# Performance work log

Hardware: AMD Instinct MI355X
Metric: run time of the kernel (lower is better)

## Reference

```python
import jax, jax.numpy as jnp
import numpy as np

B, S, D = 4, 2048, 1024
H = 16
HD = D // H

def setup_inputs() -> dict:
    key = jax.random.key(0)
    ks = jax.random.split(key, 6)
    s = 0.02
    return {
        "input_tensor": jax.random.normal(ks[0], (B, S, D), dtype=jnp.float32),
        "Wq": jax.random.normal(ks[1], (D, D), dtype=jnp.float32) * s,
        "Wk": jax.random.normal(ks[2], (D, D), dtype=jnp.float32) * s,
        "Wv": jax.random.normal(ks[3], (D, D), dtype=jnp.float32) * s,
        "Wo": jax.random.normal(ks[4], (D, D), dtype=jnp.float32) * s,
        "bo": jax.random.normal(ks[5], (D,), dtype=jnp.float32) * s,
    }

def reference(input_tensor, Wq, Wk, Wv, Wo, bo):
    b, n, _ = input_tensor.shape
    # projections (nn.Linear: x @ W.T; bias=False for qkv)
    q = jnp.einsum('bnd,ed->bne', input_tensor, Wq).reshape(b, n, H, HD).transpose(0, 2, 1, 3)
    k = jnp.einsum('bnd,ed->bne', input_tensor, Wk).reshape(b, n, H, HD).transpose(0, 2, 1, 3)
    v = jnp.einsum('bnd,ed->bne', input_tensor, Wv).reshape(b, n, H, HD).transpose(0, 2, 1, 3)
    scores = jnp.einsum('bhqd,bhkd->bhqk', q, k)  # [B,H,S,S]
    causal = jnp.triu(jnp.ones((n, n), dtype=bool), k=1)
    scores = jnp.where(causal, -jnp.inf, scores)
    weights = jax.nn.softmax(scores / jnp.sqrt(jnp.float32(HD)), axis=-1)
    ctx = jnp.einsum('bhqk,bhkd->bhqd', weights, v)  # [B,H,S,HD]
    ctx = ctx.transpose(0, 2, 1, 3).reshape(b, n, D)
    return jnp.einsum('bnd,ed->bne', ctx, Wo) + bo
```

## Files before the change

kernel.cpp:

```cpp
#include <hip/hip_runtime.h>
#include <stdint.h>

#define S_LEN 2048
#define DIM   1024
#define NH    16
#define HD    64
#define BATCH 4
#define M_ROWS (BATCH * S_LEN)

typedef __attribute__((ext_vector_type(8))) __bf16 bf16x8;
typedef __attribute__((ext_vector_type(4))) float  f32x4;

union Frag { bf16x8 v; uint4 q; };

__device__ __forceinline__ ushort f2bf(float f) {
  union { float f; unsigned u; } x; x.f = f;
  unsigned r = x.u + 0x7fffu + ((x.u >> 16) & 1u);
  return (ushort)(r >> 16);
}
__device__ __forceinline__ ushort f2bf_n(float f) {
  union { __bf16 b; ushort u; } x; x.b = (__bf16)f; return x.u;
}

__device__ __forceinline__ f32x4 mfma16(const Frag& a, const Frag& b, f32x4 c) {
  return __builtin_amdgcn_mfma_f32_16x16x32_bf16(a.v, b.v, c, 0, 0, 0);
}

__device__ __forceinline__ void gld_lds16(const ushort* g, ushort* l) {
  __builtin_amdgcn_global_load_lds(
      (__attribute__((address_space(1))) void*)g,
      (__attribute__((address_space(3))) void*)l, 16, 0, 0);
}

__global__ void cast_x_kernel(const float* __restrict__ src, ushort* __restrict__ dst) {
  int i = blockIdx.x * 256 + threadIdx.x;
  float4 f = ((const float4*)src)[i];
  ushort4 u; u.x = f2bf(f.x); u.y = f2bf(f.y); u.z = f2bf(f.z); u.w = f2bf(f.w);
  ((ushort4*)dst)[i] = u;
}

__global__ void cast_w_kernel(const float* __restrict__ w0, const float* __restrict__ w1,
                              const float* __restrict__ w2, const float* __restrict__ w3,
                              ushort* __restrict__ d0, ushort* __restrict__ d1,
                              ushort* __restrict__ d2, ushort* __restrict__ d3) {
  const float* s; ushort* d;
  int z = blockIdx.y;
  if (z == 0) { s = w0; d = d0; } else if (z == 1) { s = w1; d = d1; }
  else if (z == 2) { s = w2; d = d2; } else { s = w3; d = d3; }
  int i = blockIdx.x * 256 + threadIdx.x;
  float4 f = ((const float4*)s)[i];
  ushort4 u; u.x = f2bf(f.x); u.y = f2bf(f.y); u.z = f2bf(f.z); u.w = f2bf(f.w);
  ((ushort4*)d)[i] = u;
}

template <int MODE>
__global__ __launch_bounds__(256)
void gemm_bk64(const ushort* __restrict__ A,
               const ushort* __restrict__ B0, const ushort* __restrict__ B1,
               const ushort* __restrict__ B2,
               ushort* __restrict__ Qb, ushort* __restrict__ Kb, ushort* __restrict__ Vtb,
               float* __restrict__ outf, const float* __restrict__ bias, float scaleq) {
  __shared__ __align__(16) ushort As[128 * 64];
  __shared__ __align__(16) ushort Bs[128 * 64];
  const int K = DIM;
  int lane = threadIdx.x & 63, wave = threadIdx.x >> 6;
  int quad = lane >> 4, l15 = lane & 15;

  const int GX = (MODE == 0) ? 24 : 8;
  int lin = blockIdx.x + GX * blockIdx.y;
  int xcd = lin & 7, idx = lin >> 3;
  int by = xcd * 8 + idx / GX;
  int bx = idx % GX;

  int rowBase = by * 128;
  int wsel, colBase;
  const ushort* Bt;
  if (MODE == 0) {
    wsel = bx >> 3;
    colBase = (bx & 7) * 128;
    Bt = (wsel == 0) ? B0 : (wsel == 1) ? B1 : B2;
  } else {
    wsel = 0;
    colBase = bx * 128;
    Bt = B0;
  }
  int wm = (wave >> 1) * 64, wn = (wave & 1) * 64;

  const ushort* Ag = A + (size_t)rowBase * K;
  const ushort* Bg = Bt + (size_t)colBase * K;

  f32x4 acc[4][4];
#pragma unroll
  for (int i = 0; i < 4; i++)
#pragma unroll
    for (int j = 0; j < 4; j++) acc[i][j] = (f32x4){0.f, 0.f, 0.f, 0.f};

  for (int k0 = 0; k0 < K; k0 += 64) {
#pragma unroll
    for (int cc = 0; cc < 4; ++cc) {
      int c = wave * 4 + cc;
      int s = c * 64 + lane;
      int row = s >> 3;
      int c8 = (s & 7) ^ (row & 7);
      gld_lds16(Ag + (size_t)row * K + k0 + c8 * 8, &As[c * 512]);
      gld_lds16(Bg + (size_t)row * K + k0 + c8 * 8, &Bs[c * 512]);
    }
    __syncthreads();
    Frag af[4][2], bf[4][2];
#pragma unroll
    for (int t = 0; t < 4; t++) {
      int ar = wm + t * 16 + l15;
      int br = wn + t * 16 + l15;
#pragma unroll
      for (int kk = 0; kk < 2; kk++) {
        af[t][kk].q = *(const uint4*)&As[ar * 64 + (((kk * 4 + quad) ^ (ar & 7))) * 8];
        bf[t][kk].q = *(const uint4*)&Bs[br * 64 + (((kk * 4 + quad) ^ (br & 7))) * 8];
      }
    }
#pragma unroll
    for (int kk = 0; kk < 2; kk++)
#pragma unroll
      for (int i = 0; i < 4; i++)
#pragma unroll
        for (int j = 0; j < 4; j++) acc[i][j] = mfma16(af[i][kk], bf[j][kk], acc[i][j]);
    __syncthreads();
  }

#pragma unroll
  for (int i = 0; i < 4; i++) {
    int rowt = wm + i * 16 + quad * 4;
#pragma unroll
    for (int j = 0; j < 4; j++) {
      int e = colBase + wn + j * 16 + l15;
      if (MODE == 0) {
        if (wsel < 2) {
          ushort* dst = wsel ? Kb : Qb;
          float sc = wsel ? 1.f : scaleq;
#pragma unroll
          for (int r = 0; r < 4; r++) {
            size_t m = (size_t)(rowBase + rowt + r);
            dst[m * DIM + e] = f2bf(acc[i][j][r] * sc);
          }
        } else {
          int h = e >> 6, hd = e & 63;
          int m0 = rowBase + rowt;
          int b = m0 >> 11, s0 = m0 & (S_LEN - 1);
          ushort4 u;
          u.x = f2bf(acc[i][j][0]); u.y = f2bf(acc[i][j][1]);
          u.z = f2bf(acc[i][j][2]); u.w = f2bf(acc[i][j][3]);
          *(ushort4*)&Vtb[((size_t)((b * NH + h) * HD + hd) << 11) + s0] = u;
        }
      } else {
        float bv = bias[e];
#pragma unroll
        for (int r = 0; r < 4; r++) {
          int m = rowBase + rowt + r;
          outf[(size_t)m * DIM + e] = acc[i][j][r] + bv;
        }
      }
    }
  }
}

__global__ __launch_bounds__(256)
void flash_attn(const ushort* __restrict__ Qb, const ushort* __restrict__ Kb,
                const ushort* __restrict__ Vtb, ushort* __restrict__ Ctx) {
  __shared__ __align__(16) ushort Ks[128 * 64];
  __shared__ __align__(16) ushort Vs[64 * 128];

  int lane = threadIdx.x & 63, wave = threadIdx.x >> 6;
  int quad = lane >> 4, l15 = lane & 15;
  int bh = blockIdx.x;
  int qt = (gridDim.y - 1) - blockIdx.y;
  int q0 = qt * 128, wq0 = wave * 32;
  int b = bh >> 4, h = bh & 15;

  const ushort* Qg = Qb + (size_t)b * S_LEN * DIM + h * HD;
  const ushort* Kg = Kb + (size_t)b * S_LEN * DIM + h * HD;
  const ushort* Vh = Vtb + (size_t)bh * HD * S_LEN;

#pragma unroll
  for (int cc = 0; cc < 4; ++cc) {
    int c = wave * 4 + cc;
    int s = c * 64 + lane;
    int row = s >> 3;
    int c8 = (s & 7) ^ (row & 7);
    gld_lds16(Qg + (size_t)(q0 + row) * DIM + c8 * 8, &Ks[c * 512]);
  }
  __syncthreads();
  Frag qf[2][2];
#pragma unroll
  for (int it = 0; it < 2; ++it)
#pragma unroll
    for (int ks = 0; ks < 2; ++ks) {
      int row = wq0 + it * 16 + l15;
      int c8 = (ks * 4 + quad) ^ (row & 7);
      qf[it][ks].q = *(const uint4*)&Ks[row * 64 + c8 * 8];
    }
  __syncthreads();

  float lst[2] = {0.f, 0.f};
  f32x4 oacc[2][4];
#pragma unroll
  for (int it = 0; it < 2; ++it)
#pragma unroll
    for (int dt = 0; dt < 4; ++dt) oacc[it][dt] = (f32x4){0.f, 0.f, 0.f, 0.f};

  ushort* Pw = &Ks[wave * 2048];

  for (int kt = 0; kt <= qt; ++kt) {
#pragma unroll
    for (int cc = 0; cc < 4; ++cc) {
      int c = wave * 4 + cc;
      int s = c * 64 + lane;
      int krow = s >> 3;
      int kc8 = (s & 7) ^ (krow & 7);
      gld_lds16(Kg + (size_t)(kt * 128 + krow) * DIM + kc8 * 8, &Ks[c * 512]);
      int vrow = s >> 4;
      int vc8 = (s & 15) ^ (vrow & 15);
      gld_lds16(Vh + (size_t)vrow * S_LEN + kt * 128 + vc8 * 8, &Vs[c * 512]);
    }
    __syncthreads();

    f32x4 sacc[2][8];
#pragma unroll
    for (int jt = 0; jt < 8; ++jt) {
      int row = jt * 16 + l15;
      Frag kf0, kf1;
      kf0.q = *(const uint4*)&Ks[row * 64 + ((quad) ^ (row & 7)) * 8];
      kf1.q = *(const uint4*)&Ks[row * 64 + ((4 + quad) ^ (row & 7)) * 8];
#pragma unroll
      for (int it = 0; it < 2; ++it) {
        f32x4 a = (f32x4){0.f, 0.f, 0.f, 0.f};
        a = mfma16(kf0, qf[it][0], a);
        a = mfma16(kf1, qf[it][1], a);
        sacc[it][jt] = a;
      }
    }
    __syncthreads();

    if (kt == qt) {
#pragma unroll
      for (int it = 0; it < 2; ++it)
#pragma unroll
        for (int jt = 0; jt < 8; ++jt)
#pragma unroll
          for (int r = 0; r < 4; ++r)
            if (jt * 16 + quad * 4 + r > wq0 + it * 16 + l15)
              sacc[it][jt][r] = -1e30f;
    }

#pragma unroll
    for (int it = 0; it < 2; ++it) {
      float ps = 0.f;
#pragma unroll
      for (int jt = 0; jt < 8; ++jt) {
        float p0 = exp2f(sacc[it][jt][0]);
        float p1 = exp2f(sacc[it][jt][1]);
        float p2 = exp2f(sacc[it][jt][2]);
        float p3 = exp2f(sacc[it][jt][3]);
        ps += (p0 + p1) + (p2 + p3);
        ushort4 u; u.x = f2bf_n(p0); u.y = f2bf_n(p1); u.z = f2bf_n(p2); u.w = f2bf_n(p3);
        int cw = (jt * 4 + quad) ^ (l15 << 1);
        *(ushort4*)&Pw[l15 * 128 + cw * 4] = u;
      }
      ps += __shfl_xor(ps, 16);
      ps += __shfl_xor(ps, 32);
      lst[it] += ps;

      Frag pf[4];
#pragma unroll
      for (int ks = 0; ks < 4; ++ks) {
        int cr = (ks * 8 + quad * 2) ^ (l15 << 1);
        pf[ks].q = *(const uint4*)&Pw[l15 * 128 + cr * 4];
      }

#pragma unroll
      for (int dt = 0; dt < 4; ++dt) {
        f32x4 a = oacc[it][dt];
#pragma unroll
        for (int ks = 0; ks < 4; ++ks) {
          int row = dt * 16 + l15;
          Frag vf;
          vf.q = *(const uint4*)&Vs[row * 128 + (((ks * 4 + quad) ^ (row & 15))) * 8];
          a = mfma16(pf[ks], vf, a);
        }
        oacc[it][dt] = a;
      }
    }
    __syncthreads();
  }

#pragma unroll
  for (int it = 0; it < 2; ++it) {
    float linv = 1.f / lst[it];
    float lr[4];
#pragma unroll
    for (int r = 0; r < 4; ++r) lr[r] = __shfl(linv, quad * 4 + r);
#pragma unroll
    for (int r = 0; r < 4; ++r) {
      int qg = q0 + wq0 + it * 16 + quad * 4 + r;
      size_t base = ((size_t)(b * S_LEN + qg)) * DIM + h * HD;
#pragma unroll
      for (int dt = 0; dt < 4; ++dt)
        Ctx[base + dt * 16 + l15] = f2bf_n(oacc[it][dt][r] * lr[r]);
    }
  }
}

extern "C" void kernel_launch(void* const* d_in, const int* in_sizes, int n_in,
                              void* d_out, int out_size, void* d_ws, size_t ws_size,
                              hipStream_t stream) {
  (void)in_sizes; (void)n_in; (void)out_size; (void)ws_size;
  const float* x  = (const float*)d_in[0];
  const float* Wq = (const float*)d_in[1];
  const float* Wk = (const float*)d_in[2];
  const float* Wv = (const float*)d_in[3];
  const float* Wo = (const float*)d_in[4];
  const float* bo = (const float*)d_in[5];
  float* out = (float*)d_out;

  ushort* Xb  = (ushort*)d_ws;
  ushort* Wqb = Xb  + (size_t)M_ROWS * DIM;
  ushort* Wkb = Wqb + (size_t)DIM * DIM;
  ushort* Wvb = Wkb + (size_t)DIM * DIM;
  ushort* Wob = Wvb + (size_t)DIM * DIM;
  ushort* Qb  = Wob + (size_t)DIM * DIM;
  ushort* Kb  = Qb  + (size_t)M_ROWS * DIM;
  ushort* Vtb = Kb  + (size_t)M_ROWS * DIM;
  ushort* Ctx = Vtb + (size_t)M_ROWS * DIM;

  const float SCALE_Q = 0.18033688011112042f;

  cast_x_kernel<<<dim3(M_ROWS * DIM / 1024), 256, 0, stream>>>(x, Xb);
  cast_w_kernel<<<dim3(DIM * DIM / 1024, 4), 256, 0, stream>>>(Wq, Wk, Wv, Wo, Wqb, Wkb, Wvb, Wob);

  gemm_bk64<0><<<dim3(24, 64), 256, 0, stream>>>(Xb, Wqb, Wkb, Wvb, Qb, Kb, Vtb,
                                                 nullptr, nullptr, SCALE_Q);

  flash_attn<<<dim3(BATCH * NH, S_LEN / 128), 256, 0, stream>>>(Qb, Kb, Vtb, Ctx);

  gemm_bk64<1><<<dim3(8, 64), 256, 0, stream>>>(Ctx, Wob, nullptr, nullptr, nullptr, nullptr,
                                                nullptr, out, bo, 1.0f);
}
```

Before: 269.3 us.

## Pair causal query tiles per block, add dedicated P buffer, vectorize GEMM stores

The attention kernel now processes two query tiles per block (tile i and its mirror NQT-1-i), so every block does equal causal work; the grid is halved to match. P moves to its own padded shared buffer, which lets the mid-iteration barrier between the QK and PV phases be removed. The GEMM swaps MFMA operand order for the Q/K and output paths so each lane holds contiguous columns, allowing 4-wide vector stores and float4 bias loads. The changes trade more LDS per block and fewer blocks against better load balance and fewer synchronisations and store instructions.

```diff
diff --git a/kernel.cpp b/kernel.cpp
--- a/kernel.cpp
+++ b/kernel.cpp
@@ -7,6 +7,7 @@
 #define HD    64
 #define BATCH 4
 #define M_ROWS (BATCH * S_LEN)
+#define PSTR  136
 
 typedef __attribute__((ext_vector_type(8))) __bf16 bf16x8;
 typedef __attribute__((ext_vector_type(4))) float  f32x4;
@@ -85,6 +86,7 @@
     Bt = B0;
   }
   int wm = (wave >> 1) * 64, wn = (wave & 1) * 64;
+  bool swapT = (MODE == 1) || (wsel < 2);
 
   const ushort* Ag = A + (size_t)rowBase * K;
   const ushort* Bg = Bt + (size_t)colBase * K;
@@ -117,46 +119,67 @@
         bf[t][kk].q = *(const uint4*)&Bs[br * 64 + (((kk * 4 + quad) ^ (br & 7))) * 8];
       }
     }
-#pragma unroll
-    for (int kk = 0; kk < 2; kk++)
-#pragma unroll
-      for (int i = 0; i < 4; i++)
-#pragma unroll
-        for (int j = 0; j < 4; j++) acc[i][j] = mfma16(af[i][kk], bf[j][kk], acc[i][j]);
+    if (swapT) {
+#pragma unroll
+      for (int kk = 0; kk < 2; kk++)
+#pragma unroll
+        for (int i = 0; i < 4; i++)
+#pragma unroll
+          for (int j = 0; j < 4; j++) acc[i][j] = mfma16(bf[j][kk], af[i][kk], acc[i][j]);
+    } else {
+#pragma unroll
+      for (int kk = 0; kk < 2; kk++)
+#pragma unroll
+        for (int i = 0; i < 4; i++)
+#pragma unroll
+          for (int j = 0; j < 4; j++) acc[i][j] = mfma16(af[i][kk], bf[j][kk], acc[i][j]);
+    }
     __syncthreads();
   }
 
-#pragma unroll
-  for (int i = 0; i < 4; i++) {
-    int rowt = wm + i * 16 + quad * 4;
-#pragma unroll
-    for (int j = 0; j < 4; j++) {
-      int e = colBase + wn + j * 16 + l15;
-      if (MODE == 0) {
-        if (wsel < 2) {
-          ushort* dst = wsel ? Kb : Qb;
-          float sc = wsel ? 1.f : scaleq;
-#pragma unroll
-          for (int r = 0; r < 4; r++) {
-            size_t m = (size_t)(rowBase + rowt + r);
-            dst[m * DIM + e] = f2bf(acc[i][j][r] * sc);
-          }
-        } else {
-          int h = e >> 6, hd = e & 63;
-          int m0 = rowBase + rowt;
-          int b = m0 >> 11, s0 = m0 & (S_LEN - 1);
-          ushort4 u;
-          u.x = f2bf(acc[i][j][0]); u.y = f2bf(acc[i][j][1]);
-          u.z = f2bf(acc[i][j][2]); u.w = f2bf(acc[i][j][3]);
-          *(ushort4*)&Vtb[((size_t)((b * NH + h) * HD + hd) << 11) + s0] = u;
-        }
-      } else {
-        float bv = bias[e];
-#pragma unroll
-        for (int r = 0; r < 4; r++) {
-          int m = rowBase + rowt + r;
-          outf[(size_t)m * DIM + e] = acc[i][j][r] + bv;
-        }
+  if (MODE == 0 && wsel == 2) {
+#pragma unroll
+    for (int i = 0; i < 4; i++) {
+      int rowt = wm + i * 16 + quad * 4;
+#pragma unroll
+      for (int j = 0; j < 4; j++) {
+        int e = colBase + wn + j * 16 + l15;
+        int h = e >> 6, hd = e & 63;
+        int m0 = rowBase + rowt;
+        int b = m0 >> 11, s0 = m0 & (S_LEN - 1);
+        ushort4 u;
+        u.x = f2bf(acc[i][j][0]); u.y = f2bf(acc[i][j][1]);
+        u.z = f2bf(acc[i][j][2]); u.w = f2bf(acc[i][j][3]);
+        *(ushort4*)&Vtb[((size_t)((b * NH + h) * HD + hd) << 11) + s0] = u;
+      }
+    }
+  } else if (MODE == 0) {
+    ushort* dst = wsel ? Kb : Qb;
+    float sc = wsel ? 1.f : scaleq;
+#pragma unroll
+    for (int i = 0; i < 4; i++) {
+      size_t m = (size_t)(rowBase + wm + i * 16 + l15);
+#pragma unroll
+      for (int j = 0; j < 4; j++) {
+        int e = colBase + wn + j * 16 + quad * 4;
+        ushort4 u;
+        u.x = f2bf(acc[i][j][0] * sc); u.y = f2bf(acc[i][j][1] * sc);
+        u.z = f2bf(acc[i][j][2] * sc); u.w = f2bf(acc[i][j][3] * sc);
+        *(ushort4*)&dst[m * DIM + e] = u;
+      }
+    }
+  } else {
+#pragma unroll
+    for (int i = 0; i < 4; i++) {
+      size_t m = (size_t)(rowBase + wm + i * 16 + l15);
+#pragma unroll
+      for (int j = 0; j < 4; j++) {
+        int e = colBase + wn + j * 16 + quad * 4;
+        float4 bv = *(const float4*)&bias[e];
+        float4 o;
+        o.x = acc[i][j][0] + bv.x; o.y = acc[i][j][1] + bv.y;
+        o.z = acc[i][j][2] + bv.z; o.w = acc[i][j][3] + bv.w;
+        *(float4*)&outf[m * DIM + e] = o;
       }
     }
   }
@@ -167,144 +190,149 @@
                 const ushort* __restrict__ Vtb, ushort* __restrict__ Ctx) {
   __shared__ __align__(16) ushort Ks[128 * 64];
   __shared__ __align__(16) ushort Vs[64 * 128];
+  __shared__ __align__(16) ushort Ps[4][16 * PSTR];
 
   int lane = threadIdx.x & 63, wave = threadIdx.x >> 6;
   int quad = lane >> 4, l15 = lane & 15;
   int bh = blockIdx.x;
-  int qt = (gridDim.y - 1) - blockIdx.y;
-  int q0 = qt * 128, wq0 = wave * 32;
+  int wq0 = wave * 32;
   int b = bh >> 4, h = bh & 15;
 
   const ushort* Qg = Qb + (size_t)b * S_LEN * DIM + h * HD;
   const ushort* Kg = Kb + (size_t)b * S_LEN * DIM + h * HD;
   const ushort* Vh = Vtb + (size_t)bh * HD * S_LEN;
-
-#pragma unroll
-  for (int cc = 0; cc < 4; ++cc) {
-    int c = wave * 4 + cc;
-    int s = c * 64 + lane;
-    int row = s >> 3;
-    int c8 = (s & 7) ^ (row & 7);
-    gld_lds16(Qg + (size_t)(q0 + row) * DIM + c8 * 8, &Ks[c * 512]);
-  }
-  __syncthreads();
-  Frag qf[2][2];
-#pragma unroll
-  for (int it = 0; it < 2; ++it)
-#pragma unroll
-    for (int ks = 0; ks < 2; ++ks) {
-      int row = wq0 + it * 16 + l15;
-      int c8 = (ks * 4 + quad) ^ (row & 7);
-      qf[it][ks].q = *(const uint4*)&Ks[row * 64 + c8 * 8];
-    }
-  __syncthreads();
-
-  float lst[2] = {0.f, 0.f};
-  f32x4 oacc[2][4];
-#pragma unroll
-  for (int it = 0; it < 2; ++it)
-#pragma unroll
-    for (int dt = 0; dt < 4; ++dt) oacc[it][dt] = (f32x4){0.f, 0.f, 0.f, 0.f};
-
-  ushort* Pw = &Ks[wave * 2048];
-
-  for (int kt = 0; kt <= qt; ++kt) {
+  ushort* Pw = Ps[wave];
+
+  const int NQT = S_LEN / 128;
+
+#pragma unroll 1
+  for (int pass = 0; pass < 2; ++pass) {
+    int qt = pass ? blockIdx.y : (NQT - 1 - blockIdx.y);
+    int q0 = qt * 128;
+
 #pragma unroll
     for (int cc = 0; cc < 4; ++cc) {
       int c = wave * 4 + cc;
       int s = c * 64 + lane;
-      int krow = s >> 3;
-      int kc8 = (s & 7) ^ (krow & 7);
-      gld_lds16(Kg + (size_t)(kt * 128 + krow) * DIM + kc8 * 8, &Ks[c * 512]);
-      int vrow = s >> 4;
-      int vc8 = (s & 15) ^ (vrow & 15);
-      gld_lds16(Vh + (size_t)vrow * S_LEN + kt * 128 + vc8 * 8, &Vs[c * 512]);
-    }
-    __syncthreads();
-
-    f32x4 sacc[2][8];
-#pragma unroll
-    for (int jt = 0; jt < 8; ++jt) {
-      int row = jt * 16 + l15;
-      Frag kf0, kf1;
-      kf0.q = *(const uint4*)&Ks[row * 64 + ((quad) ^ (row & 7)) * 8];
-      kf1.q = *(const uint4*)&Ks[row * 64 + ((4 + quad) ^ (row & 7)) * 8];
+      int row = s >> 3;
+      int c8 = (s & 7) ^ (row & 7);
+      gld_lds16(Qg + (size_t)(q0 + row) * DIM + c8 * 8, &Ks[c * 512]);
+    }
+    __syncthreads();
+    Frag qf[2][2];
+#pragma unroll
+    for (int it = 0; it < 2; ++it)
+#pragma unroll
+      for (int ks = 0; ks < 2; ++ks) {
+        int row = wq0 + it * 16 + l15;
+        int c8 = (ks * 4 + quad) ^ (row & 7);
+        qf[it][ks].q = *(const uint4*)&Ks[row * 64 + c8 * 8];
+      }
+    __syncthreads();
+
+    float lst[2] = {0.f, 0.f};
+    f32x4 oacc[2][4];
+#pragma unroll
+    for (int it = 0; it < 2; ++it)
+#pragma unroll
+      for (int dt = 0; dt < 4; ++dt) oacc[it][dt] = (f32x4){0.f, 0.f, 0.f, 0.f};
+
+#pragma unroll 1
+    for (int kt = 0; kt <= qt; ++kt) {
+#pragma unroll
+      for (int cc = 0; cc < 4; ++cc) {
+        int c = wave * 4 + cc;
+        int s = c * 64 + lane;
+        int krow = s >> 3;
+        int kc8 = (s & 7) ^ (krow & 7);
+        gld_lds16(Kg + (size_t)(kt * 128 + krow) * DIM + kc8 * 8, &Ks[c * 512]);
+        int vrow = s >> 4;
+        int vc8 = (s & 15) ^ (vrow & 15);
+        gld_lds16(Vh + (size_t)vrow * S_LEN + kt * 128 + vc8 * 8, &Vs[c * 512]);
+      }
+      __syncthreads();
+
+      f32x4 sacc[2][8];
+#pragma unroll
+      for (int jt = 0; jt < 8; ++jt) {
+        int row = jt * 16 + l15;
+        Frag kf0, kf1;
+        kf0.q = *(const uint4*)&Ks[row * 64 + ((quad) ^ (row & 7)) * 8];
+        kf1.q = *(const uint4*)&Ks[row * 64 + ((4 + quad) ^ (row & 7)) * 8];
+#pragma unroll
+        for (int it = 0; it < 2; ++it) {
+          f32x4 a = (f32x4){0.f, 0.f, 0.f, 0.f};
+          a = mfma16(kf0, qf[it][0], a);
+          a = mfma16(kf1, qf[it][1], a);
+          sacc[it][jt] = a;
+        }
+      }
+
+      if (kt == qt) {
+#pragma unroll
+        for (int it = 0; it < 2; ++it)
+#pragma unroll
+          for (int jt = 0; jt < 8; ++jt)
+#pragma unroll
+            for (int r = 0; r < 4; ++r)
+              if (jt * 16 + quad * 4 + r > wq0 + it * 16 + l15)
+                sacc[it][jt][r] = -1e30f;
+      }
+
 #pragma unroll
       for (int it = 0; it < 2; ++it) {
-        f32x4 a = (f32x4){0.f, 0.f, 0.f, 0.f};
-        a = mfma16(kf0, qf[it][0], a);
-        a = mfma16(kf1, qf[it][1], a);
-        sacc[it][jt] = a;
-      }
-    }
-    __syncthreads();
-
-    if (kt == qt) {
-#pragma unroll
-      for (int it = 0; it < 2; ++it)
-#pragma unroll
-        for (int jt = 0; jt < 8; ++jt)
-#pragma unroll
-          for (int r = 0; r < 4; ++r)
-            if (jt * 16 + quad * 4 + r > wq0 + it * 16 + l15)
-              sacc[it][jt][r] = -1e30f;
+        float ps = 0.f;
+#pragma unroll
+        for (int jt = 0; jt < 8; ++jt) {
+          float p0 = exp2f(sacc[it][jt][0]);
+          float p1 = exp2f(sacc[it][jt][1]);
+          float p2 = exp2f(sacc[it][jt][2]);
+          float p3 = exp2f(sacc[it][jt][3]);
+          ps += (p0 + p1) + (p2 + p3);
+          ushort4 u; u.x = f2bf_n(p0); u.y = f2bf_n(p1); u.z = f2bf_n(p2); u.w = f2bf_n(p3);
+          *(ushort4*)&Pw[l15 * PSTR + jt * 16 + quad * 4] = u;
+        }
+        ps += __shfl_xor(ps, 16);
+        ps += __shfl_xor(ps, 32);
+        lst[it] += ps;
+
+        Frag pf[4];
+#pragma unroll
+        for (int ks = 0; ks < 4; ++ks)
+          pf[ks].q = *(const uint4*)&Pw[l15 * PSTR + ks * 32 + quad * 8];
+
+#pragma unroll
+        for (int dt = 0; dt < 4; ++dt) {
+          f32x4 a = oacc[it][dt];
+#pragma unroll
+          for (int ks = 0; ks < 4; ++ks) {
+            int row = dt * 16 + l15;
+            Frag vf;
+            vf.q = *(const uint4*)&Vs[row * 128 + (((ks * 4 + quad) ^ (row & 15))) * 8];
+            a = mfma16(pf[ks], vf, a);
+          }
+          oacc[it][dt] = a;
+        }
+      }
+      __syncthreads();
     }
 
 #pragma unroll
     for (int it = 0; it < 2; ++it) {
-      float ps = 0.f;
-#pragma unroll
-      for (int jt = 0; jt < 8; ++jt) {
-        float p0 = exp2f(sacc[it][jt][0]);
-        float p1 = exp2f(sacc[it][jt][1]);
-        float p2 = exp2f(sacc[it][jt][2]);
-        float p3 = exp2f(sacc[it][jt][3]);
-        ps += (p0 + p1) + (p2 + p3);
-        ushort4 u; u.x = f2bf_n(p0); u.y = f2bf_n(p1); u.z = f2bf_n(p2); u.w = f2bf_n(p3);
-        int cw = (jt * 4 + quad) ^ (l15 << 1);
-        *(ushort4*)&Pw[l15 * 128 + cw * 4] = u;
-      }
-      ps += __shfl_xor(ps, 16);
-      ps += __shfl_xor(ps, 32);
-      lst[it] += ps;
-
-      Frag pf[4];
-#pragma unroll
-      for (int ks = 0; ks < 4; ++ks) {
-        int cr = (ks * 8 + quad * 2) ^ (l15 << 1);
-        pf[ks].q = *(const uint4*)&Pw[l15 * 128 + cr * 4];
-      }
-
-#pragma unroll
-      for (int dt = 0; dt < 4; ++dt) {
-        f32x4 a = oacc[it][dt];
-#pragma unroll
-        for (int ks = 0; ks < 4; ++ks) {
-          int row = dt * 16 + l15;
-          Frag vf;
-          vf.q = *(const uint4*)&Vs[row * 128 + (((ks * 4 + quad) ^ (row & 15))) * 8];
-          a = mfma16(pf[ks], vf, a);
-        }
-        oacc[it][dt] = a;
-      }
-    }
-    __syncthreads();
-  }
-
-#pragma unroll
-  for (int it = 0; it < 2; ++it) {
-    float linv = 1.f / lst[it];
-    float lr[4];
-#pragma unroll
-    for (int r = 0; r < 4; ++r) lr[r] = __shfl(linv, quad * 4 + r);
-#pragma unroll
-    for (int r = 0; r < 4; ++r) {
-      int qg = q0 + wq0 + it * 16 + quad * 4 + r;
-      size_t base = ((size_t)(b * S_LEN + qg)) * DIM + h * HD;
-#pragma unroll
-      for (int dt = 0; dt < 4; ++dt)
-        Ctx[base + dt * 16 + l15] = f2bf_n(oacc[it][dt][r] * lr[r]);
-    }
+      float linv = 1.f / lst[it];
+      float lr[4];
+#pragma unroll
+      for (int r = 0; r < 4; ++r) lr[r] = __shfl(linv, quad * 4 + r);
+#pragma unroll
+      for (int r = 0; r < 4; ++r) {
+        int qg = q0 + wq0 + it * 16 + quad * 4 + r;
+        size_t base = ((size_t)(b * S_LEN + qg)) * DIM + h * HD;
+#pragma unroll
+        for (int dt = 0; dt < 4; ++dt)
+          Ctx[base + dt * 16 + l15] = f2bf_n(oacc[it][dt][r] * lr[r]);
+      }
+    }
+    __syncthreads();
   }
 }
 
@@ -338,7 +366,7 @@
   gemm_bk64<0><<<dim3(24, 64), 256, 0, stream>>>(Xb, Wqb, Wkb, Wvb, Qb, Kb, Vtb,
                                                  nullptr, nullptr, SCALE_Q);
 
-  flash_attn<<<dim3(BATCH * NH, S_LEN / 128), 256, 0, stream>>>(Qb, Kb, Vtb, Ctx);
+  flash_attn<<<dim3(BATCH * NH, S_LEN / 256), 256, 0, stream>>>(Qb, Kb, Vtb, Ctx);
 
   gemm_bk64<1><<<dim3(8, 64), 256, 0, stream>>>(Ctx, Wob, nullptr, nullptr, nullptr, nullptr,
                                                 nullptr, out, bo, 1.0f);
```

After: 276.1 us. 2.5% more time.
